# Optimization experiments

Measured on AMD Instinct MI355X. Metric: run time of the kernel, lower is better.

Reference implementation:

```python
import jax, jax.numpy as jnp
import numpy as np

T = 10.0           # distillation temperature (init arg T)
LOSS_WEIGHT = 1.0  # module-level loss_weight (init arg)
EPS_STD = 1e-07
EPS_RATIO = 1e-08

ROWS, BINS = 1048576, 17  # (4*N, n+1), n = 16


def setup_inputs() -> dict:
    key = jax.random.key(0)
    k1, k2, k3 = jax.random.split(key, 3)
    pred = jax.random.normal(k1, (ROWS, BINS), dtype=jnp.float32)
    soft_label = jax.random.normal(k2, (ROWS, BINS), dtype=jnp.float32)
    weight = jax.random.uniform(k3, (ROWS,), dtype=jnp.float32)
    return {"pred": pred, "soft_label": soft_label, "weight": weight}


def _normalize(logit):
    # torch .std() is unbiased (ddof=1)
    mean = jnp.mean(logit, axis=-1, keepdims=True)
    stdv = jnp.std(logit, axis=-1, keepdims=True, ddof=1)
    return (logit - mean) / (EPS_STD + stdv)


def reference(pred, soft_label, weight):
    soft = jax.lax.stop_gradient(soft_label)  # detach_target=True

    # kd_loss_ls with logit_stand=True
    ls = _normalize(pred)
    lt = _normalize(soft)
    log_p_student = jax.nn.log_softmax(ls / T, axis=1)
    log_p_teacher = jax.nn.log_softmax(lt / T, axis=1)
    p_teacher = jnp.exp(log_p_teacher)
    # F.kl_div(log_pred, target, 'none') = target * (log(target) - log_pred)
    loss_ls = jnp.mean(jnp.sum(p_teacher * (log_p_teacher - log_p_student), axis=1)) * (T * T)

    # sum_distributions_loop on target = softmax(soft_label) -- batched full conv1d
    target = jax.nn.softmax(soft, axis=1)            # (4N, bins)
    n_rows, bins = target.shape
    N = n_rows // 4
    t = target.reshape(N, 4, bins)
    top, bottom, left, right = t[:, 0], t[:, 1], t[:, 2], t[:, 3]
    # pad+flip+conv1d in torch == true full convolution, length 2*bins-1 = 2n+1
    conv_full = jax.vmap(lambda a, b: jnp.convolve(a, b, mode='full'))
    sum_lr = conv_full(left, right)                   # (N, 2n+1)
    sum_tb = conv_full(top, bottom)                   # (N, 2n+1)
    target_ratio = sum_lr / (sum_tb + EPS_RATIO)

    # weighted_loss wrapper: loss * weight, then 'mean' reduction; outer * loss_weight
    loss = LOSS_WEIGHT * jnp.mean(loss_ls * weight)
    return loss, target_ratio
```

## Files before the change

### kernel.cpp

```cpp
#include <hip/hip_runtime.h>

#define ROWS 1048576
#define BINS 17
#define RPB 64
#define NBLK (ROWS / RPB)
#define GPB (RPB / 4)
#define CONV_N 33

template <bool PART>
__global__ __launch_bounds__(64, 4) void kd_main(
    const float* __restrict__ pred,
    const float* __restrict__ soft,
    const float* __restrict__ weight,
    float* __restrict__ out,
    float* __restrict__ ws)
{
    __shared__ float sA[RPB * BINS];
    __shared__ float sB[RPB * BINS];
    const int tid = threadIdx.x;
    const long long base = (long long)blockIdx.x * (RPB * BINS);

    const float4* p4 = reinterpret_cast<const float4*>(pred + base);
    const float4* q4 = reinterpret_cast<const float4*>(soft + base);
    float4* a4 = reinterpret_cast<float4*>(sA);
    float4* b4 = reinterpret_cast<float4*>(sB);
#pragma unroll
    for (int k = 0; k < 4; ++k) {
        a4[k * 64 + tid] = p4[k * 64 + tid];
        b4[k * 64 + tid] = q4[k * 64 + tid];
    }
    if (tid < 16) {
        a4[256 + tid] = p4[256 + tid];
        b4[256 + tid] = q4[256 + tid];
    }
    const float w = weight[blockIdx.x * RPB + tid];
    __syncthreads();

    float x[BINS], y[BINS];
    float sx = 0.f, sy = 0.f, xmx = -1e30f, ymx = -1e30f;
#pragma unroll
    for (int j = 0; j < BINS; ++j) {
        x[j] = sA[tid * BINS + j];
        y[j] = sB[tid * BINS + j];
        sx += x[j]; sy += y[j];
        xmx = fmaxf(xmx, x[j]); ymx = fmaxf(ymx, y[j]);
    }
    const float mx = sx * (1.0f / BINS);
    const float my = sy * (1.0f / BINS);

    float vx = 0.f, vy = 0.f;
#pragma unroll
    for (int j = 0; j < BINS; ++j) {
        const float dx = x[j] - mx; vx = fmaf(dx, dx, vx);
        const float dy = y[j] - my; vy = fmaf(dy, dy, vy);
    }
    const float invsx = 0.1f / (1e-7f + sqrtf(vx * (1.0f / (BINS - 1))));
    const float invsy = 0.1f / (1e-7f + sqrtf(vy * (1.0f / (BINS - 1))));
    const float amax = (xmx - mx) * invsx;
    const float bmax = (ymx - my) * invsy;

    float sea = 0.f, seb = 0.f, ts = 0.f;
#pragma unroll
    for (int j = 0; j < BINS; ++j) {
        sea += __expf((x[j] - mx) * invsx - amax);
        seb += __expf((y[j] - my) * invsy - bmax);
        ts  += __expf(y[j] - ymx);
    }
    const float la = __logf(sea);
    const float lb = __logf(seb);
    const float invseb = 1.0f / seb;
    const float invts  = 1.0f / ts;

    float kl = 0.f;
#pragma unroll
    for (int j = 0; j < BINS; ++j) {
        const float aj = (x[j] - mx) * invsx - amax;
        const float bj = (y[j] - my) * invsy - bmax;
        kl = fmaf(__expf(bj), (bj - lb) - (aj - la), kl);
    }
    kl *= invseb;

#pragma unroll
    for (int j = 0; j < BINS; ++j)
        sA[tid * BINS + j] = __expf(y[j] - ymx) * invts;

    float k2 = kl, w2 = w;
#pragma unroll
    for (int off = 32; off >= 1; off >>= 1) {
        k2 += __shfl_down(k2, off, 64);
        w2 += __shfl_down(w2, off, 64);
    }

    __syncthreads();

    float* sR = sB;

    if (tid < 2 * GPB) {
        const int g = tid >> 1;
        const int R = 4 * g + ((tid & 1) ? 0 : 2);
        float f[2 * BINS];
        const float2* pr = reinterpret_cast<const float2*>(&sA[R * BINS]);
#pragma unroll
        for (int i = 0; i < BINS; ++i) {
            const float2 v = pr[i];
            f[2 * i] = v.x; f[2 * i + 1] = v.y;
        }
        float accv[CONV_N];
#pragma unroll
        for (int j = 0; j < CONV_N; ++j) accv[j] = 0.f;
#pragma unroll
        for (int k = 0; k < BINS; ++k)
#pragma unroll
            for (int m = 0; m < BINS; ++m)
                accv[k + m] = fmaf(f[k], f[BINS + m], accv[k + m]);

#pragma unroll
        for (int j = 0; j < CONV_N; ++j) {
            const float o = __shfl_down(accv[j], 1, 64);
            if ((tid & 1) == 0)
                sR[g * CONV_N + j] = accv[j] / (o + 1e-8f);
        }
    }
    __syncthreads();

    const long long ob = 1 + (long long)blockIdx.x * (GPB * CONV_N);
#pragma unroll
    for (int i = 0; i < 8; ++i)
        out[ob + i * 64 + tid] = sR[i * 64 + tid];
    if (tid < 16) out[ob + 512 + tid] = sR[512 + tid];

    if (tid == 0) {
        if (PART) {
            ws[blockIdx.x]        = k2;
            ws[NBLK + blockIdx.x] = w2;
        } else {
            atomicAdd(&ws[0], k2);
            atomicAdd(&ws[1], w2);
        }
    }
}

template <bool PART>
__global__ __launch_bounds__(1024) void kd_reduce(
    const float* __restrict__ ws, float* __restrict__ out)
{
    if (!PART) {
        if (threadIdx.x == 0)
            out[0] = 100.0f * (ws[0] * (1.0f / ROWS)) * (ws[1] * (1.0f / ROWS));
        return;
    }
    __shared__ float red[32];
    const int tid = threadIdx.x;
    const float4* k4 = reinterpret_cast<const float4*>(ws);
    const float4* w4 = reinterpret_cast<const float4*>(ws + NBLK);
    float ks = 0.f, wsum = 0.f;
#pragma unroll
    for (int i = 0; i < 4; ++i) {
        const float4 a = k4[i * 1024 + tid];
        const float4 b = w4[i * 1024 + tid];
        ks += (a.x + a.y) + (a.z + a.w);
        wsum += (b.x + b.y) + (b.z + b.w);
    }
#pragma unroll
    for (int off = 32; off >= 1; off >>= 1) {
        ks += __shfl_down(ks, off, 64);
        wsum += __shfl_down(wsum, off, 64);
    }
    if ((tid & 63) == 0) {
        red[(tid >> 6) * 2 + 0] = ks;
        red[(tid >> 6) * 2 + 1] = wsum;
    }
    __syncthreads();
    if (tid == 0) {
        float K = 0.f, W = 0.f;
#pragma unroll
        for (int i = 0; i < 16; ++i) { K += red[2 * i]; W += red[2 * i + 1]; }
        out[0] = 100.0f * (K * (1.0f / ROWS)) * (W * (1.0f / ROWS));
    }
}

extern "C" void kernel_launch(void* const* d_in, const int* in_sizes, int n_in,
                              void* d_out, int out_size, void* d_ws, size_t ws_size,
                              hipStream_t stream)
{
    const float* pred   = (const float*)d_in[0];
    const float* soft   = (const float*)d_in[1];
    const float* weight = (const float*)d_in[2];
    float* out = (float*)d_out;
    float* ws  = (float*)d_ws;

    if (ws_size >= (size_t)(2 * NBLK) * sizeof(float)) {
        kd_main<true><<<NBLK, RPB, 0, stream>>>(pred, soft, weight, out, ws);
        kd_reduce<true><<<1, 1024, 0, stream>>>(ws, out);
    } else {
        hipMemsetAsync(ws, 0, 2 * sizeof(float), stream);
        kd_main<false><<<NBLK, RPB, 0, stream>>>(pred, soft, weight, out, ws);
        kd_reduce<false><<<1, 1024, 0, stream>>>(ws, out);
    }
}
```

Before: 183.5 us.

## Stage pred and soft through one shared buffer and fuse softmax/KL passes

Loads both inputs into registers first, then stages pred and soft in turn through a single shared array, roughly halving LDS per block. The exponent, sum and KL accumulations are merged into one pass with split accumulators and an algebraic simplification of the KL term. It also caches exp(y-max) for reuse in the target softmax. This adds extra barriers and register pressure in exchange for less LDS and fewer transcendental evaluations.

```diff
diff --git a/kernel.cpp b/kernel.cpp
--- a/kernel.cpp
+++ b/kernel.cpp
@@ -16,73 +16,105 @@
     float* __restrict__ ws)
 {
     __shared__ float sA[RPB * BINS];
-    __shared__ float sB[RPB * BINS];
+    __shared__ float sR[GPB * CONV_N];
     const int tid = threadIdx.x;
     const long long base = (long long)blockIdx.x * (RPB * BINS);
 
     const float4* p4 = reinterpret_cast<const float4*>(pred + base);
     const float4* q4 = reinterpret_cast<const float4*>(soft + base);
+    float4 P[5] = {}, Q[5] = {};
+#pragma unroll
+    for (int k = 0; k < 4; ++k) {
+        P[k] = p4[k * 64 + tid];
+        Q[k] = q4[k * 64 + tid];
+    }
+    if (tid < 16) { P[4] = p4[256 + tid]; Q[4] = q4[256 + tid]; }
+    const float w = weight[blockIdx.x * RPB + tid];
+
     float4* a4 = reinterpret_cast<float4*>(sA);
-    float4* b4 = reinterpret_cast<float4*>(sB);
-#pragma unroll
-    for (int k = 0; k < 4; ++k) {
-        a4[k * 64 + tid] = p4[k * 64 + tid];
-        b4[k * 64 + tid] = q4[k * 64 + tid];
-    }
-    if (tid < 16) {
-        a4[256 + tid] = p4[256 + tid];
-        b4[256 + tid] = q4[256 + tid];
-    }
-    const float w = weight[blockIdx.x * RPB + tid];
-    __syncthreads();
-
-    float x[BINS], y[BINS];
-    float sx = 0.f, sy = 0.f, xmx = -1e30f, ymx = -1e30f;
+#pragma unroll
+    for (int k = 0; k < 4; ++k) a4[k * 64 + tid] = P[k];
+    if (tid < 16) a4[256 + tid] = P[4];
+    __syncthreads();
+
+    float x[BINS];
+#pragma unroll
+    for (int j = 0; j < BINS; ++j) x[j] = sA[tid * BINS + j];
+
+    float s0 = 0.f, s1 = 0.f, m0 = -1e30f, m1 = -1e30f;
+#pragma unroll
+    for (int j = 0; j < 16; j += 2) {
+        s0 += x[j];     m0 = fmaxf(m0, x[j]);
+        s1 += x[j + 1]; m1 = fmaxf(m1, x[j + 1]);
+    }
+    const float mx  = (s0 + s1 + x[16]) * (1.0f / BINS);
+    const float xmx = fmaxf(fmaxf(m0, m1), x[16]);
+
+    float v0 = 0.f, v1 = 0.f;
+#pragma unroll
+    for (int j = 0; j < 16; j += 2) {
+        const float d0 = x[j] - mx;     v0 = fmaf(d0, d0, v0);
+        const float d1 = x[j + 1] - mx; v1 = fmaf(d1, d1, v1);
+    }
+    const float dx16 = x[16] - mx;
+    const float vx = fmaf(dx16, dx16, v0 + v1);
+    const float invsx = 0.1f / (1e-7f + sqrtf(vx * (1.0f / (BINS - 1))));
+    const float amax = (xmx - mx) * invsx;
+    const float ca = -mx * invsx - amax;
+
+    __syncthreads();
+#pragma unroll
+    for (int k = 0; k < 4; ++k) a4[k * 64 + tid] = Q[k];
+    if (tid < 16) a4[256 + tid] = Q[4];
+    __syncthreads();
+
+    float y[BINS];
+#pragma unroll
+    for (int j = 0; j < BINS; ++j) y[j] = sA[tid * BINS + j];
+
+    s0 = 0.f; s1 = 0.f; m0 = -1e30f; m1 = -1e30f;
+#pragma unroll
+    for (int j = 0; j < 16; j += 2) {
+        s0 += y[j];     m0 = fmaxf(m0, y[j]);
+        s1 += y[j + 1]; m1 = fmaxf(m1, y[j + 1]);
+    }
+    const float my  = (s0 + s1 + y[16]) * (1.0f / BINS);
+    const float ymx = fmaxf(fmaxf(m0, m1), y[16]);
+
+    v0 = 0.f; v1 = 0.f;
+#pragma unroll
+    for (int j = 0; j < 16; j += 2) {
+        const float d0 = y[j] - my;     v0 = fmaf(d0, d0, v0);
+        const float d1 = y[j + 1] - my; v1 = fmaf(d1, d1, v1);
+    }
+    const float dy16 = y[16] - my;
+    const float vy = fmaf(dy16, dy16, v0 + v1);
+    const float invsy = 0.1f / (1e-7f + sqrtf(vy * (1.0f / (BINS - 1))));
+    const float bmax = (ymx - my) * invsy;
+    const float cb = -my * invsy - bmax;
+
+    float ey[BINS];
+    float sea0 = 0.f, sea1 = 0.f, seb0 = 0.f, seb1 = 0.f;
+    float ts0 = 0.f, ts1 = 0.f, D0 = 0.f, D1 = 0.f;
 #pragma unroll
     for (int j = 0; j < BINS; ++j) {
-        x[j] = sA[tid * BINS + j];
-        y[j] = sB[tid * BINS + j];
-        sx += x[j]; sy += y[j];
-        xmx = fmaxf(xmx, x[j]); ymx = fmaxf(ymx, y[j]);
-    }
-    const float mx = sx * (1.0f / BINS);
-    const float my = sy * (1.0f / BINS);
-
-    float vx = 0.f, vy = 0.f;
-#pragma unroll
-    for (int j = 0; j < BINS; ++j) {
-        const float dx = x[j] - mx; vx = fmaf(dx, dx, vx);
-        const float dy = y[j] - my; vy = fmaf(dy, dy, vy);
-    }
-    const float invsx = 0.1f / (1e-7f + sqrtf(vx * (1.0f / (BINS - 1))));
-    const float invsy = 0.1f / (1e-7f + sqrtf(vy * (1.0f / (BINS - 1))));
-    const float amax = (xmx - mx) * invsx;
-    const float bmax = (ymx - my) * invsy;
-
-    float sea = 0.f, seb = 0.f, ts = 0.f;
-#pragma unroll
-    for (int j = 0; j < BINS; ++j) {
-        sea += __expf((x[j] - mx) * invsx - amax);
-        seb += __expf((y[j] - my) * invsy - bmax);
-        ts  += __expf(y[j] - ymx);
-    }
-    const float la = __logf(sea);
-    const float lb = __logf(seb);
-    const float invseb = 1.0f / seb;
-    const float invts  = 1.0f / ts;
-
-    float kl = 0.f;
-#pragma unroll
-    for (int j = 0; j < BINS; ++j) {
-        const float aj = (x[j] - mx) * invsx - amax;
-        const float bj = (y[j] - my) * invsy - bmax;
-        kl = fmaf(__expf(bj), (bj - lb) - (aj - la), kl);
-    }
-    kl *= invseb;
+        const float aj = fmaf(x[j], invsx, ca);
+        const float bj = fmaf(y[j], invsy, cb);
+        const float eb = __expf(bj);
+        const float ea = __expf(aj);
+        ey[j] = __expf(y[j] - ymx);
+        if (j & 1) { seb1 += eb; sea1 += ea; ts1 += ey[j]; D1 = fmaf(eb, bj - aj, D1); }
+        else       { seb0 += eb; sea0 += ea; ts0 += ey[j]; D0 = fmaf(eb, bj - aj, D0); }
+    }
+    const float seb = seb0 + seb1;
+    const float sea = sea0 + sea1;
+    const float ts  = ts0 + ts1;
+    const float kl  = (D0 + D1) / seb - __logf(seb) + __logf(sea);
+    const float invts = 1.0f / ts;
 
 #pragma unroll
     for (int j = 0; j < BINS; ++j)
-        sA[tid * BINS + j] = __expf(y[j] - ymx) * invts;
+        sA[tid * BINS + j] = ey[j] * invts;
 
     float k2 = kl, w2 = w;
 #pragma unroll
@@ -92,8 +124,6 @@
     }
 
     __syncthreads();
-
-    float* sR = sB;
 
     if (tid < 2 * GPB) {
         const int g = tid >> 1;
```

Measured after the change: 210.3 us. +14.6%, slower.
